# Kernel tuning notes

Hardware: AMD Instinct MI355X
Metric: run time of the kernel (lower is better)

## Reference

```python
import jax, jax.numpy as jnp
import numpy as np

N, IN_DIM, OUT_DIM, HEADS = 4096, 128, 32, 4
EDGE_PROB = 0.015  # ~61 neighbors/node on average


def setup_inputs() -> dict:
    key = jax.random.key(0)
    k1, k2, k3, k4 = jax.random.split(key, 4)
    x = jax.random.normal(k1, (N, IN_DIM), dtype=jnp.float32)
    adj = (jax.random.uniform(k2, (N, N)) < EDGE_PROB).astype(jnp.float32)
    adj = jnp.maximum(adj, jnp.eye(N, dtype=jnp.float32))  # self loops so softmax is never all-masked
    # nn.Linear(in_dim, out_dim*heads, bias=False): weight stored here as [in, out]
    W = jax.random.normal(k3, (IN_DIM, OUT_DIM * HEADS), dtype=jnp.float32) / np.sqrt(IN_DIM).astype(np.float32)
    # nn.Linear(2*out_dim, 1, bias=False) -> a single [2*out_dim] vector shared across heads
    a = jax.random.normal(k4, (2 * OUT_DIM,), dtype=jnp.float32) / np.sqrt(2 * OUT_DIM).astype(np.float32)
    return {"x": x, "adj": adj, "W": W, "a": a}


def reference(x, adj, W, a):
    n = x.shape[0]
    xp = (x @ W).reshape(n, HEADS, OUT_DIM)  # [N, H, D]
    # Original builds concat([x_expanded, x_j_expanded])[i,j] = [x[j] || x[i]] and applies
    # a linear map. Since attn is linear, scores decompose: e[i,j,h] = a1.x[j,h] + a2.x[i,h].
    a_j, a_i = a[:OUT_DIM], a[OUT_DIM:]
    s_j = jnp.einsum('nhd,d->nh', xp, a_j)  # contribution of column node j
    s_i = jnp.einsum('nhd,d->nh', xp, a_i)  # contribution of row node i
    scale = jnp.float32(1.0 / np.sqrt(OUT_DIM))
    e = (s_i[:, None, :] + s_j[None, :, :]) * scale  # [N, N, H]
    e = e + ((1.0 - adj) * jnp.float32(-1e9))[:, :, None]
    att = jax.nn.softmax(e, axis=1)  # softmax over dim=1 (neighbors j), as in original
    out = jnp.einsum('ijh,jhd->ihd', att, xp)  # attention-weighted neighbor aggregation
    return out.reshape(n, HEADS * OUT_DIM)
```

## Files before the change

### kernel.cpp

```cpp
#include <hip/hip_runtime.h>

#define N_NODES 4096
#define IN_DIM  128
#define OUT_DIM 32
#define HEADS   4
#define FDIM    128
#define K1_ROWS 8

__global__ __launch_bounds__(256) void gat_proj(const float* __restrict__ x,
                                                const float* __restrict__ W,
                                                const float* __restrict__ a,
                                                float* __restrict__ Y,
                                                float* __restrict__ Eg) {
    __shared__ float xs[K1_ROWS * IN_DIM];
    __shared__ float eS[K1_ROWS][HEADS];
    const int t    = threadIdx.x;
    const int row0 = blockIdx.x * K1_ROWS;

    ((float4*)xs)[t] = ((const float4*)(x + (size_t)row0 * IN_DIM))[t];
    __syncthreads();

    const int c  = t & 127;
    const int rg = t >> 7;
    const float* xb = xs + (rg * 4) * IN_DIM;

    float acc0 = 0.f, acc1 = 0.f, acc2 = 0.f, acc3 = 0.f;
#pragma unroll 4
    for (int k0 = 0; k0 < IN_DIM; k0 += 4) {
        const float w0 = W[(k0 + 0) * FDIM + c];
        const float w1 = W[(k0 + 1) * FDIM + c];
        const float w2 = W[(k0 + 2) * FDIM + c];
        const float w3 = W[(k0 + 3) * FDIM + c];
        const float4 x0 = *(const float4*)(xb + 0 * IN_DIM + k0);
        const float4 x1 = *(const float4*)(xb + 1 * IN_DIM + k0);
        const float4 x2 = *(const float4*)(xb + 2 * IN_DIM + k0);
        const float4 x3 = *(const float4*)(xb + 3 * IN_DIM + k0);
        acc0 = fmaf(x0.x, w0, fmaf(x0.y, w1, fmaf(x0.z, w2, fmaf(x0.w, w3, acc0))));
        acc1 = fmaf(x1.x, w0, fmaf(x1.y, w1, fmaf(x1.z, w2, fmaf(x1.w, w3, acc1))));
        acc2 = fmaf(x2.x, w0, fmaf(x2.y, w1, fmaf(x2.z, w2, fmaf(x2.w, w3, acc2))));
        acc3 = fmaf(x3.x, w0, fmaf(x3.y, w1, fmaf(x3.z, w2, fmaf(x3.w, w3, acc3))));
    }

    const int rb = rg * 4;
    __syncthreads();
    xs[(rb + 0) * FDIM + c] = acc0;
    xs[(rb + 1) * FDIM + c] = acc1;
    xs[(rb + 2) * FDIM + c] = acc2;
    xs[(rb + 3) * FDIM + c] = acc3;
    __syncthreads();

    if (t < K1_ROWS * HEADS) {
        const int r = t >> 2, h = t & 3;
        const float4* xr = (const float4*)(xs + r * FDIM + h * OUT_DIM);
        const float4* aj = (const float4*)a;
        float vj = 0.f;
#pragma unroll
        for (int q = 0; q < 8; ++q) {
            const float4 xv = xr[q], a0 = aj[q];
            vj += xv.x * a0.x + xv.y * a0.y + xv.z * a0.z + xv.w * a0.w;
        }
        const float e = __expf(vj * 0.17677669529663687f);
        eS[r][h] = e;
        Eg[(row0 + r) * HEADS + h] = e;
    }
    __syncthreads();

    const int h = c >> 5;
    Y[(size_t)(row0 + rb + 0) * FDIM + c] = acc0 * eS[rb + 0][h];
    Y[(size_t)(row0 + rb + 1) * FDIM + c] = acc1 * eS[rb + 1][h];
    Y[(size_t)(row0 + rb + 2) * FDIM + c] = acc2 * eS[rb + 2][h];
    Y[(size_t)(row0 + rb + 3) * FDIM + c] = acc3 * eS[rb + 3][h];
}

__global__ __launch_bounds__(256, 4) void gat_sum(const float* __restrict__ adj,
                                                  const float* __restrict__ Y,
                                                  const float* __restrict__ E,
                                                  float* __restrict__ out) {
    const int tid  = threadIdx.x;
    const int wv   = tid >> 6;
    const int lane = tid & 63;
    const int row  = blockIdx.x * 4 + wv;
    const int hm   = lane >> 4;

    __shared__ int elist[4][N_NODES / 4];
    int* seg = elist[wv];

    const float4* arow = (const float4*)(adj + (size_t)row * N_NODES);
    float4 v[16];
#pragma unroll
    for (int c = 0; c < 16; ++c) v[c] = arow[c * 64 + lane];

    const unsigned long long lt = (1ULL << lane) - 1ULL;
    int base = 0;
#pragma unroll
    for (int c = 0; c < 16; ++c) {
        const int cb = c * 256 + lane * 4;
        const float vals[4] = {v[c].x, v[c].y, v[c].z, v[c].w};
#pragma unroll
        for (int m = 0; m < 4; ++m) {
            const unsigned long long mk = __ballot(vals[m] != 0.f);
            if (vals[m] != 0.f) seg[base + __popcll(mk & lt)] = cb + m;
            base += __popcll(mk);
        }
    }
    const int cnt = base;

    const float2* Y2 = (const float2*)Y;
    const float*  Eh = E + hm;
    float ax0 = 0.f, ay0 = 0.f, z0 = 0.f;
    float ax1 = 0.f, ay1 = 0.f, z1 = 0.f;
    float ax2 = 0.f, ay2 = 0.f, z2 = 0.f;
    float ax3 = 0.f, ay3 = 0.f, z3 = 0.f;

    int e = 0;
    for (; e + 8 <= cnt; e += 8) {
        const int4 ja = *(const int4*)&seg[e];
        const int4 jb = *(const int4*)&seg[e + 4];
        const float2 y0 = Y2[(size_t)ja.x * 64 + lane];
        const float2 y1 = Y2[(size_t)ja.y * 64 + lane];
        const float2 y2 = Y2[(size_t)ja.z * 64 + lane];
        const float2 y3 = Y2[(size_t)ja.w * 64 + lane];
        const float2 y4 = Y2[(size_t)jb.x * 64 + lane];
        const float2 y5 = Y2[(size_t)jb.y * 64 + lane];
        const float2 y6 = Y2[(size_t)jb.z * 64 + lane];
        const float2 y7 = Y2[(size_t)jb.w * 64 + lane];
        const float e0 = Eh[(size_t)ja.x * 4];
        const float e1 = Eh[(size_t)ja.y * 4];
        const float e2 = Eh[(size_t)ja.z * 4];
        const float e3 = Eh[(size_t)ja.w * 4];
        const float e4 = Eh[(size_t)jb.x * 4];
        const float e5 = Eh[(size_t)jb.y * 4];
        const float e6 = Eh[(size_t)jb.z * 4];
        const float e7 = Eh[(size_t)jb.w * 4];
        ax0 += y0.x; ay0 += y0.y; z0 += e0;
        ax1 += y1.x; ay1 += y1.y; z1 += e1;
        ax2 += y2.x; ay2 += y2.y; z2 += e2;
        ax3 += y3.x; ay3 += y3.y; z3 += e3;
        ax0 += y4.x; ay0 += y4.y; z0 += e4;
        ax1 += y5.x; ay1 += y5.y; z1 += e5;
        ax2 += y6.x; ay2 += y6.y; z2 += e6;
        ax3 += y7.x; ay3 += y7.y; z3 += e7;
    }
    for (; e < cnt; ++e) {
        const int j = seg[e];
        const float2 yv = Y2[(size_t)j * 64 + lane];
        ax0 += yv.x; ay0 += yv.y; z0 += Eh[(size_t)j * 4];
    }

    const float z = (z0 + z1) + (z2 + z3);
    const float invZ = 1.0f / z;
    float2 o;
    o.x = ((ax0 + ax1) + (ax2 + ax3)) * invZ;
    o.y = ((ay0 + ay1) + (ay2 + ay3)) * invZ;
    ((float2*)out)[(size_t)row * 64 + lane] = o;
}

extern "C" void kernel_launch(void* const* d_in, const int* in_sizes, int n_in,
                              void* d_out, int out_size, void* d_ws, size_t ws_size,
                              hipStream_t stream) {
    const float* x   = (const float*)d_in[0];
    const float* adj = (const float*)d_in[1];
    const float* W   = (const float*)d_in[2];
    const float* a   = (const float*)d_in[3];
    float* out = (float*)d_out;

    float* Y = (float*)d_ws;
    float* E = Y + (size_t)N_NODES * FDIM;

    gat_proj<<<N_NODES / K1_ROWS, 256, 0, stream>>>(x, W, a, Y, E);
    gat_sum<<<N_NODES / 4, 256, 0, stream>>>(adj, Y, E, out);
}
```

Measured before the change: 33.57 us.

## Store projected features as bf16 and split each adjacency row across two waves

The projection kernel now writes the exp-weighted features as packed bf16 pairs, which halves the bytes gathered per neighbour in the aggregation kernel. The aggregation kernel gives each row to two waves, each scanning half the adjacency row. The halves are combined through shared memory, the gather loop is unrolled to 16 neighbours, and occupancy is raised through a smaller fixed-capacity edge list with a fallback path. This reduces precision of the aggregated features to bf16 and adds an extra block-wide sync and a combine step.

```diff
diff --git a/kernel.cpp b/kernel.cpp
--- a/kernel.cpp
+++ b/kernel.cpp
@@ -6,11 +6,19 @@
 #define HEADS   4
 #define FDIM    128
 #define K1_ROWS 8
+#define CAP     512
+
+static __device__ __forceinline__ unsigned bf16pack(float a, float b) {
+    unsigned ua = __float_as_uint(a), ub = __float_as_uint(b);
+    ua = (ua + 0x7FFFu + ((ua >> 16) & 1u)) >> 16;
+    ub = (ub + 0x7FFFu + ((ub >> 16) & 1u)) >> 16;
+    return ua | (ub << 16);
+}
 
 __global__ __launch_bounds__(256) void gat_proj(const float* __restrict__ x,
                                                 const float* __restrict__ W,
                                                 const float* __restrict__ a,
-                                                float* __restrict__ Y,
+                                                unsigned* __restrict__ Ybf,
                                                 float* __restrict__ Eg) {
     __shared__ float xs[K1_ROWS * IN_DIM];
     __shared__ float eS[K1_ROWS][HEADS];
@@ -65,94 +73,161 @@
     }
     __syncthreads();
 
-    const int h = c >> 5;
-    Y[(size_t)(row0 + rb + 0) * FDIM + c] = acc0 * eS[rb + 0][h];
-    Y[(size_t)(row0 + rb + 1) * FDIM + c] = acc1 * eS[rb + 1][h];
-    Y[(size_t)(row0 + rb + 2) * FDIM + c] = acc2 * eS[rb + 2][h];
-    Y[(size_t)(row0 + rb + 3) * FDIM + c] = acc3 * eS[rb + 3][h];
-}
-
-__global__ __launch_bounds__(256, 4) void gat_sum(const float* __restrict__ adj,
-                                                  const float* __restrict__ Y,
+#pragma unroll
+    for (int q = 0; q < 2; ++q) {
+        const int idx = t + 256 * q;
+        const int r   = idx >> 6;
+        const int cp  = idx & 63;
+        const float e = eS[r][cp >> 4];
+        const float a0 = xs[r * FDIM + 2 * cp]     * e;
+        const float a1 = xs[r * FDIM + 2 * cp + 1] * e;
+        Ybf[(size_t)(row0 + r) * 64 + cp] = bf16pack(a0, a1);
+    }
+}
+
+__global__ __launch_bounds__(256, 6) void gat_sum(const float* __restrict__ adj,
+                                                  const unsigned* __restrict__ Ybf,
                                                   const float* __restrict__ E,
                                                   float* __restrict__ out) {
     const int tid  = threadIdx.x;
     const int wv   = tid >> 6;
     const int lane = tid & 63;
-    const int row  = blockIdx.x * 4 + wv;
+    const int row  = blockIdx.x * 2 + (wv >> 1);
+    const int half = wv & 1;
     const int hm   = lane >> 4;
 
-    __shared__ int elist[4][N_NODES / 4];
-    int* seg = elist[wv];
-
-    const float4* arow = (const float4*)(adj + (size_t)row * N_NODES);
-    float4 v[16];
-#pragma unroll
-    for (int c = 0; c < 16; ++c) v[c] = arow[c * 64 + lane];
+    __shared__ int    seg_s[4][CAP];
+    __shared__ float4 part_s[4][64];
+
+    const float4* arow = (const float4*)(adj + (size_t)row * N_NODES) + half * 512;
+    float4 v[8];
+#pragma unroll
+    for (int c = 0; c < 8; ++c) v[c] = arow[c * 64 + lane];
 
     const unsigned long long lt = (1ULL << lane) - 1ULL;
+    int* seg = seg_s[wv];
     int base = 0;
 #pragma unroll
-    for (int c = 0; c < 16; ++c) {
-        const int cb = c * 256 + lane * 4;
+    for (int c = 0; c < 8; ++c) {
+        const int cb = half * 2048 + c * 256 + lane * 4;
         const float vals[4] = {v[c].x, v[c].y, v[c].z, v[c].w};
 #pragma unroll
         for (int m = 0; m < 4; ++m) {
             const unsigned long long mk = __ballot(vals[m] != 0.f);
-            if (vals[m] != 0.f) seg[base + __popcll(mk & lt)] = cb + m;
+            const int pos = base + __popcll(mk & lt);
+            if (vals[m] != 0.f && pos < CAP) seg[pos] = cb + m;
             base += __popcll(mk);
         }
     }
     const int cnt = base;
 
-    const float2* Y2 = (const float2*)Y;
-    const float*  Eh = E + hm;
+    const float* Eh = E + hm;
     float ax0 = 0.f, ay0 = 0.f, z0 = 0.f;
     float ax1 = 0.f, ay1 = 0.f, z1 = 0.f;
     float ax2 = 0.f, ay2 = 0.f, z2 = 0.f;
     float ax3 = 0.f, ay3 = 0.f, z3 = 0.f;
 
-    int e = 0;
-    for (; e + 8 <= cnt; e += 8) {
-        const int4 ja = *(const int4*)&seg[e];
-        const int4 jb = *(const int4*)&seg[e + 4];
-        const float2 y0 = Y2[(size_t)ja.x * 64 + lane];
-        const float2 y1 = Y2[(size_t)ja.y * 64 + lane];
-        const float2 y2 = Y2[(size_t)ja.z * 64 + lane];
-        const float2 y3 = Y2[(size_t)ja.w * 64 + lane];
-        const float2 y4 = Y2[(size_t)jb.x * 64 + lane];
-        const float2 y5 = Y2[(size_t)jb.y * 64 + lane];
-        const float2 y6 = Y2[(size_t)jb.z * 64 + lane];
-        const float2 y7 = Y2[(size_t)jb.w * 64 + lane];
-        const float e0 = Eh[(size_t)ja.x * 4];
-        const float e1 = Eh[(size_t)ja.y * 4];
-        const float e2 = Eh[(size_t)ja.z * 4];
-        const float e3 = Eh[(size_t)ja.w * 4];
-        const float e4 = Eh[(size_t)jb.x * 4];
-        const float e5 = Eh[(size_t)jb.y * 4];
-        const float e6 = Eh[(size_t)jb.z * 4];
-        const float e7 = Eh[(size_t)jb.w * 4];
-        ax0 += y0.x; ay0 += y0.y; z0 += e0;
-        ax1 += y1.x; ay1 += y1.y; z1 += e1;
-        ax2 += y2.x; ay2 += y2.y; z2 += e2;
-        ax3 += y3.x; ay3 += y3.y; z3 += e3;
-        ax0 += y4.x; ay0 += y4.y; z0 += e4;
-        ax1 += y5.x; ay1 += y5.y; z1 += e5;
-        ax2 += y6.x; ay2 += y6.y; z2 += e6;
-        ax3 += y7.x; ay3 += y7.y; z3 += e7;
-    }
-    for (; e < cnt; ++e) {
-        const int j = seg[e];
-        const float2 yv = Y2[(size_t)j * 64 + lane];
-        ax0 += yv.x; ay0 += yv.y; z0 += Eh[(size_t)j * 4];
-    }
-
-    const float z = (z0 + z1) + (z2 + z3);
-    const float invZ = 1.0f / z;
-    float2 o;
-    o.x = ((ax0 + ax1) + (ax2 + ax3)) * invZ;
-    o.y = ((ay0 + ay1) + (ay2 + ay3)) * invZ;
-    ((float2*)out)[(size_t)row * 64 + lane] = o;
+#define ACC(ch, u, ev)                                                        \
+    {                                                                         \
+        ax##ch += __uint_as_float((u) << 16);                                 \
+        ay##ch += __uint_as_float((u) & 0xFFFF0000u);                         \
+        z##ch  += (ev);                                                       \
+    }
+
+    if (__builtin_expect(cnt <= CAP, 1)) {
+        int e = 0;
+        for (; e + 16 <= cnt; e += 16) {
+            const int4 ja = *(const int4*)&seg[e];
+            const int4 jb = *(const int4*)&seg[e + 4];
+            const int4 jc = *(const int4*)&seg[e + 8];
+            const int4 jd = *(const int4*)&seg[e + 12];
+            const unsigned u0  = Ybf[(size_t)ja.x * 64 + lane];
+            const unsigned u1  = Ybf[(size_t)ja.y * 64 + lane];
+            const unsigned u2  = Ybf[(size_t)ja.z * 64 + lane];
+            const unsigned u3  = Ybf[(size_t)ja.w * 64 + lane];
+            const unsigned u4  = Ybf[(size_t)jb.x * 64 + lane];
+            const unsigned u5  = Ybf[(size_t)jb.y * 64 + lane];
+            const unsigned u6  = Ybf[(size_t)jb.z * 64 + lane];
+            const unsigned u7  = Ybf[(size_t)jb.w * 64 + lane];
+            const unsigned u8  = Ybf[(size_t)jc.x * 64 + lane];
+            const unsigned u9  = Ybf[(size_t)jc.y * 64 + lane];
+            const unsigned u10 = Ybf[(size_t)jc.z * 64 + lane];
+            const unsigned u11 = Ybf[(size_t)jc.w * 64 + lane];
+            const unsigned u12 = Ybf[(size_t)jd.x * 64 + lane];
+            const unsigned u13 = Ybf[(size_t)jd.y * 64 + lane];
+            const unsigned u14 = Ybf[(size_t)jd.z * 64 + lane];
+            const unsigned u15 = Ybf[(size_t)jd.w * 64 + lane];
+            const float e0  = Eh[(size_t)ja.x * 4];
+            const float e1  = Eh[(size_t)ja.y * 4];
+            const float e2  = Eh[(size_t)ja.z * 4];
+            const float e3  = Eh[(size_t)ja.w * 4];
+            const float e4  = Eh[(size_t)jb.x * 4];
+            const float e5  = Eh[(size_t)jb.y * 4];
+            const float e6  = Eh[(size_t)jb.z * 4];
+            const float e7  = Eh[(size_t)jb.w * 4];
+            const float e8  = Eh[(size_t)jc.x * 4];
+            const float e9  = Eh[(size_t)jc.y * 4];
+            const float e10 = Eh[(size_t)jc.z * 4];
+            const float e11 = Eh[(size_t)jc.w * 4];
+            const float e12 = Eh[(size_t)jd.x * 4];
+            const float e13 = Eh[(size_t)jd.y * 4];
+            const float e14 = Eh[(size_t)jd.z * 4];
+            const float e15 = Eh[(size_t)jd.w * 4];
+            ACC(0, u0,  e0)  ACC(1, u1,  e1)  ACC(2, u2,  e2)  ACC(3, u3,  e3)
+            ACC(0, u4,  e4)  ACC(1, u5,  e5)  ACC(2, u6,  e6)  ACC(3, u7,  e7)
+            ACC(0, u8,  e8)  ACC(1, u9,  e9)  ACC(2, u10, e10) ACC(3, u11, e11)
+            ACC(0, u12, e12) ACC(1, u13, e13) ACC(2, u14, e14) ACC(3, u15, e15)
+        }
+        for (; e + 4 <= cnt; e += 4) {
+            const int4 ja = *(const int4*)&seg[e];
+            const unsigned u0 = Ybf[(size_t)ja.x * 64 + lane];
+            const unsigned u1 = Ybf[(size_t)ja.y * 64 + lane];
+            const unsigned u2 = Ybf[(size_t)ja.z * 64 + lane];
+            const unsigned u3 = Ybf[(size_t)ja.w * 64 + lane];
+            const float e0 = Eh[(size_t)ja.x * 4];
+            const float e1 = Eh[(size_t)ja.y * 4];
+            const float e2 = Eh[(size_t)ja.z * 4];
+            const float e3 = Eh[(size_t)ja.w * 4];
+            ACC(0, u0, e0) ACC(1, u1, e1) ACC(2, u2, e2) ACC(3, u3, e3)
+        }
+        for (; e < cnt; ++e) {
+            const int j = seg[e];
+            const unsigned u = Ybf[(size_t)j * 64 + lane];
+            ACC(0, u, Eh[(size_t)j * 4])
+        }
+    } else {
+#pragma unroll
+        for (int c = 0; c < 8; ++c) {
+            const float vals[4] = {v[c].x, v[c].y, v[c].z, v[c].w};
+#pragma unroll
+            for (int m = 0; m < 4; ++m) {
+                unsigned long long mask = __ballot(vals[m] != 0.f);
+                while (mask) {
+                    const int b = __builtin_ctzll(mask);
+                    mask &= mask - 1ULL;
+                    const int j = half * 2048 + c * 256 + b * 4 + m;
+                    const unsigned u = Ybf[(size_t)j * 64 + lane];
+                    ACC(0, u, Eh[(size_t)j * 4])
+                }
+            }
+        }
+    }
+#undef ACC
+
+    part_s[wv][lane] = make_float4((ax0 + ax1) + (ax2 + ax3),
+                                   (ay0 + ay1) + (ay2 + ay3),
+                                   (z0 + z1) + (z2 + z3), 0.f);
+    __syncthreads();
+
+    if ((wv & 1) == 0) {
+        const float4 pa = part_s[wv][lane];
+        const float4 pb = part_s[wv + 1][lane];
+        const float invZ = 1.0f / (pa.z + pb.z);
+        float2 o;
+        o.x = (pa.x + pb.x) * invZ;
+        o.y = (pa.y + pb.y) * invZ;
+        ((float2*)out)[(size_t)row * 64 + lane] = o;
+    }
 }
 
 extern "C" void kernel_launch(void* const* d_in, const int* in_sizes, int n_in,
@@ -164,9 +239,9 @@
     const float* a   = (const float*)d_in[3];
     float* out = (float*)d_out;
 
-    float* Y = (float*)d_ws;
-    float* E = Y + (size_t)N_NODES * FDIM;
-
-    gat_proj<<<N_NODES / K1_ROWS, 256, 0, stream>>>(x, W, a, Y, E);
-    gat_sum<<<N_NODES / 4, 256, 0, stream>>>(adj, Y, E, out);
-}
+    unsigned* Ybf = (unsigned*)d_ws;
+    float*    E   = (float*)(Ybf + (size_t)N_NODES * 64);
+
+    gat_proj<<<N_NODES / K1_ROWS, 256, 0, stream>>>(x, W, a, Ybf, E);
+    gat_sum<<<N_NODES / 2, 256, 0, stream>>>(adj, Ybf, E, out);
+}
```

Result: faster. 29.47 us (-12.2%).
